# Kernel optimization log

Measured on AMD Instinct MI355X. Metric: run time of the kernel, lower is better.

Reference implementation:

```python
import jax, jax.numpy as jnp
import numpy as np

B, S, H, NH = 2, 2048, 1024, 16
HD = H // NH  # head_dim = 64
ROPE_BASE = 10000.0


def _rope(x):
    # x: [B, NH, S, HD]; LLaMA-style half-split rotary embedding
    s, d = x.shape[2], x.shape[3]
    inv_freq = 1.0 / (ROPE_BASE ** (jnp.arange(0, d, 2, dtype=jnp.float32) / d))  # [d/2]
    ang = jnp.arange(s, dtype=jnp.float32)[:, None] * inv_freq[None, :]            # [S, d/2]
    cos, sin = jnp.cos(ang), jnp.sin(ang)
    x1, x2 = x[..., : d // 2], x[..., d // 2:]
    return jnp.concatenate([x1 * cos - x2 * sin, x1 * sin + x2 * cos], axis=-1)


def setup_inputs() -> dict:
    key = jax.random.key(0)
    ks = jax.random.split(key, 9)
    hidden_states = jax.random.normal(ks[0], (B, S, H), dtype=jnp.float32)
    # causal mask: True = attend
    causal = jnp.tril(jnp.ones((S, S), dtype=bool))
    attention_mask = jnp.broadcast_to(causal[None, None, :, :], (B, 1, S, S))
    std = 0.02
    wq = jax.random.normal(ks[1], (H, NH * HD), dtype=jnp.float32) * std
    wk = jax.random.normal(ks[2], (H, NH * HD), dtype=jnp.float32) * std
    wv = jax.random.normal(ks[3], (H, NH * HD), dtype=jnp.float32) * std
    wo = jax.random.normal(ks[4], (NH * HD, H), dtype=jnp.float32) * std
    bq = jnp.zeros((NH * HD,), dtype=jnp.float32)
    bk = jnp.zeros((NH * HD,), dtype=jnp.float32)
    bv = jnp.zeros((NH * HD,), dtype=jnp.float32)
    bo = jnp.zeros((H,), dtype=jnp.float32)
    return {"hidden_states": hidden_states, "attention_mask": attention_mask,
            "wq": wq, "bq": bq, "wk": wk, "bk": bk, "wv": wv, "bv": bv,
            "wo": wo, "bo": bo}


def _split_heads(x):
    b, s, _ = x.shape
    return jnp.transpose(x.reshape(b, s, NH, HD), (0, 2, 1, 3))


def reference(hidden_states, attention_mask, wq, bq, wk, bk, wv, bv, wo, bo):
    q = _split_heads(hidden_states @ wq + bq)  # [B,NH,S,HD]
    k = _split_heads(hidden_states @ wk + bk)
    v = _split_heads(hidden_states @ wv + bv)
    q = _rope(q)
    k = _rope(k)
    scores = jnp.einsum('bhqd,bhkd->bhqk', q, k) / jnp.sqrt(jnp.float32(HD))
    scores = jnp.where(attention_mask, scores, jnp.float32(-1e9))
    weights = jax.nn.softmax(scores, axis=-1)
    attn = jnp.einsum('bhqk,bhkv->bhqv', weights, v)  # [B,NH,S,HD]
    attn = jnp.transpose(attn, (0, 2, 1, 3)).reshape(hidden_states.shape[0], attn.shape[2], H)
    return attn @ wo + bo
```

## Files before the change

kernel.cpp:

```cpp
#include <hip/hip_runtime.h>
#include <math.h>

typedef short bf16x8 __attribute__((ext_vector_type(8)));
typedef short bf16x4 __attribute__((ext_vector_type(4)));
typedef float f32x4  __attribute__((ext_vector_type(4)));

__device__ __forceinline__ unsigned short f2bf(float f) {
    union { float f; unsigned u; } v; v.f = f;
    unsigned r = v.u + 0x7FFFu + ((v.u >> 16) & 1u);
    return (unsigned short)(r >> 16);
}

__device__ __forceinline__ unsigned cvt_pk_bf16(float a, float b) {
    unsigned r;
    asm("v_cvt_pk_bf16_f32 %0, %1, %2" : "=v"(r) : "v"(a), "v"(b));
    return r;
}

#define GLDS16(gp, lp) __builtin_amdgcn_global_load_lds( \
    (const __attribute__((address_space(1))) void*)(gp), \
    (__attribute__((address_space(3))) void*)(lp), 16, 0, 0)


__global__ __launch_bounds__(256)
void prep(const float* __restrict__ X, unsigned short* __restrict__ Xb,
          const float* __restrict__ w0, const float* __restrict__ w1,
          const float* __restrict__ w2, const float* __restrict__ w3,
          unsigned short* o0, unsigned short* o1,
          unsigned short* o2, unsigned short* o3)
{
    const int z = blockIdx.z;
    if (z >= 4) {
        const int lb = (z - 4) * 256 + blockIdx.y * 16 + blockIdx.x;
        const size_t t = (size_t)lb * 256 + threadIdx.x;
        const float4 a = *(const float4*)(X + t * 8);
        const float4 b = *(const float4*)(X + t * 8 + 4);
        unsigned short u[8] = { f2bf(a.x), f2bf(a.y), f2bf(a.z), f2bf(a.w),
                                f2bf(b.x), f2bf(b.y), f2bf(b.z), f2bf(b.w) };
        *(int4*)(Xb + t * 8) = *(int4*)u;
        return;
    }
    const float* W; unsigned short* O;
    switch (z) {
        case 0: W = w0; O = o0; break;
        case 1: W = w1; O = o1; break;
        case 2: W = w2; O = o2; break;
        default: W = w3; O = o3; break;
    }
    __shared__ float T[64][65];
    const int tid = threadIdx.x;
    const int n0 = blockIdx.x * 64, k0 = blockIdx.y * 64;
    #pragma unroll
    for (int i = 0; i < 4; i++) {
        const int k = (tid >> 4) + i * 16, n4 = (tid & 15) * 4;
        const float4 v = *(const float4*)(W + (size_t)(k0 + k) * 1024 + n0 + n4);
        T[k][n4] = v.x; T[k][n4+1] = v.y; T[k][n4+2] = v.z; T[k][n4+3] = v.w;
    }
    __syncthreads();
    if (z == 3) {
        #pragma unroll
        for (int i = 0; i < 4; i++) {
            const int n = (tid >> 4) + i * 16, k4 = (tid & 15) * 4;
            unsigned short u[4];
            #pragma unroll
            for (int j = 0; j < 4; j++) {
                const int q = k4 + j;
                const int p = (q & 3) * 16 + (q >> 2);
                const int d = (p & 3) * 16 + (p >> 2);
                u[j] = f2bf(T[d][n]);
            }
            *(int2*)(O + (size_t)(n0 + n) * 1024 + k0 + k4) = *(int2*)u;
        }
    } else {
        #pragma unroll
        for (int i = 0; i < 4; i++) {
            const int n = (tid >> 4) + i * 16, k4 = (tid & 15) * 4;
            unsigned short u[4] = { f2bf(T[k4][n]), f2bf(T[k4+1][n]),
                                    f2bf(T[k4+2][n]), f2bf(T[k4+3][n]) };
            *(int2*)(O + (size_t)(n0 + n) * 1024 + k0 + k4) = *(int2*)u;
        }
    }
}

__global__ __launch_bounds__(256)
void qkv_gemm(const unsigned short* __restrict__ Xb,
              const unsigned short* __restrict__ Wtq, const unsigned short* __restrict__ Wtk,
              const unsigned short* __restrict__ Wtv,
              const float* __restrict__ bq, const float* __restrict__ bk,
              const float* __restrict__ bv,
              unsigned short* __restrict__ Qb, unsigned short* __restrict__ Kb,
              unsigned short* __restrict__ Vtb)
{
    const unsigned short* Wt; const float* bias; unsigned short* Out;
    const int z = blockIdx.z;
    if (z == 0)      { Wt = Wtq; bias = bq; Out = Qb; }
    else if (z == 1) { Wt = Wtk; bias = bk; Out = Kb; }
    else             { Wt = Wtv; bias = bv; Out = Vtb; }

    __shared__ unsigned short Sh[16384];
    unsigned short* T = Sh;

    const int tid = threadIdx.x, lane = tid & 63, w = tid >> 6;
    const int quad = lane >> 4, c = lane & 15;
    const int wr = w >> 1, wc = w & 1;
    const int m0 = blockIdx.x * 128, n0 = blockIdx.y * 128;
    const int srow = lane >> 2;
    const int scol = ((lane & 3) ^ ((lane >> 3) & 3)) * 8;
    const int sA = (quad ^ ((c >> 1) & 3)) * 8;

    f32x4 acc[4][4];
    #pragma unroll
    for (int i = 0; i < 4; i++)
        #pragma unroll
        for (int j = 0; j < 4; j++) acc[i][j] = (f32x4){0.f, 0.f, 0.f, 0.f};

    #pragma unroll
    for (int j = 0; j < 2; j++) {
        const int r = w * 32 + j * 16;
        GLDS16(Xb + (size_t)(m0 + r + srow) * 1024 + 0 + scol, &Sh[r * 32]);
        GLDS16(Wt + (size_t)(n0 + r + srow) * 1024 + 0 + scol, &Sh[4096 + r * 32]);
    }
    __syncthreads();

    int cur = 0;
    for (int t = 0; t < 32; ++t) {
        if (t + 1 < 32) {
            const int kn = (t + 1) * 32;
            unsigned short* An = Sh + (cur ^ 1) * 8192;
            unsigned short* Bn = An + 4096;
            #pragma unroll
            for (int j = 0; j < 2; j++) {
                const int r = w * 32 + j * 16;
                GLDS16(Xb + (size_t)(m0 + r + srow) * 1024 + kn + scol, &An[r * 32]);
                GLDS16(Wt + (size_t)(n0 + r + srow) * 1024 + kn + scol, &Bn[r * 32]);
            }
        }
        const unsigned short* As = Sh + cur * 8192;
        const unsigned short* Bs = As + 4096;
        bf16x8 af[4], bf[4];
        #pragma unroll
        for (int rt = 0; rt < 4; rt++)
            af[rt] = *(const bf16x8*)&As[(wr * 64 + rt * 16 + c) * 32 + sA];
        #pragma unroll
        for (int nt = 0; nt < 4; nt++)
            bf[nt] = *(const bf16x8*)&Bs[(wc * 64 + nt * 16 + c) * 32 + sA];
        #pragma unroll
        for (int rt = 0; rt < 4; rt++)
            #pragma unroll
            for (int nt = 0; nt < 4; nt++)
                acc[rt][nt] = __builtin_amdgcn_mfma_f32_16x16x32_bf16(af[rt], bf[nt], acc[rt][nt], 0, 0, 0);
        __syncthreads();
        cur ^= 1;
    }

    float bv4[4];
    #pragma unroll
    for (int nt = 0; nt < 4; nt++) bv4[nt] = bias[n0 + wc * 64 + nt * 16 + c];

    if (z == 2) {
        const int b = m0 >> 11, sb = m0 & 2047;
        const int hgbase = n0 >> 6;
        #pragma unroll
        for (int h = 0; h < 2; h++) {
            if (wc == h) {
                #pragma unroll
                for (int rt = 0; rt < 4; rt++)
                    #pragma unroll
                    for (int reg = 0; reg < 4; reg++) {
                        const int s = wr * 64 + rt * 16 + quad * 4 + reg;
                        unsigned short u[4];
                        #pragma unroll
                        for (int nt = 0; nt < 4; nt++)
                            u[nt] = f2bf(acc[rt][nt][reg] + bv4[nt]);
                        *(int2*)&T[s * 72 + c * 4] = *(int2*)u;
                    }
            }
            __syncthreads();
            const int p = tid >> 2, s8 = (tid & 3) * 32;
            unsigned short* dstb = Vtb + ((size_t)(b * 16 + hgbase + h) * 64 + p) * 2048 + sb;
            #pragma unroll
            for (int jj = 0; jj < 32; jj += 8) {
                unsigned short u[8];
                #pragma unroll
                for (int j = 0; j < 8; j++) u[j] = T[(s8 + jj + j) * 72 + p];
                *(int4*)(dstb + s8 + jj) = *(int4*)u;
            }
            __syncthreads();
        }
        return;
    }

    const float kLn = 9.210340371976184f / 32.0f;
    const float TWO_PI_INV = 0.15915494309189535f;
    const float rv0 = expf(-(float)c * kLn) * TWO_PI_INV;
    const float rv1 = expf(-(float)(c + 16) * kLn) * TWO_PI_INV;
    const float qscale = (z == 0) ? 0.125f : 1.0f;

    #pragma unroll
    for (int rt = 0; rt < 4; rt++) {
        #pragma unroll
        for (int reg = 0; reg < 4; reg++) {
            const int m = m0 + wr * 64 + rt * 16 + quad * 4 + reg;
            const int b = m >> 11, s = m & 2047;
            float x0 = acc[rt][0][reg] + bv4[0];
            float x1 = acc[rt][1][reg] + bv4[1];
            float x2 = acc[rt][2][reg] + bv4[2];
            float x3 = acc[rt][3][reg] + bv4[3];
            float r0 = (float)s * rv0;  r0 -= floorf(r0);
            float r1 = (float)s * rv1;  r1 -= floorf(r1);
            const float sn0 = __builtin_amdgcn_sinf(r0);
            const float cs0 = __builtin_amdgcn_cosf(r0);
            const float sn1 = __builtin_amdgcn_sinf(r1);
            const float cs1 = __builtin_amdgcn_cosf(r1);
            const float y0 = (x0 * cs0 - x2 * sn0) * qscale;
            const float y2 = (x0 * sn0 + x2 * cs0) * qscale;
            const float y1 = (x1 * cs1 - x3 * sn1) * qscale;
            const float y3 = (x1 * sn1 + x3 * cs1) * qscale;
            const int h = (n0 + wc * 64) >> 6;
            unsigned short u[4] = { f2bf(y0), f2bf(y1), f2bf(y2), f2bf(y3) };
            unsigned short* dst = Out + ((size_t)(b * 16 + h) * 2048 + s) * 64;
            *(int2*)(dst + c * 4) = *(int2*)u;
        }
    }
}

__global__ __launch_bounds__(256)
void out_gemm(const unsigned short* __restrict__ Ab, const unsigned short* __restrict__ Wto,
              const float* __restrict__ bo, float* __restrict__ Out)
{
    __shared__ unsigned short As[64 * 32];
    __shared__ unsigned short Bs[128 * 32];
    const int tid = threadIdx.x, lane = tid & 63, w = tid >> 6;
    const int quad = lane >> 4, c = lane & 15;
    const int wr = w >> 1, wc = w & 1;
    const int m0 = blockIdx.x * 64, n0 = blockIdx.y * 128;
    const int srow = lane >> 2, scol = (lane & 3) * 8;

    f32x4 acc[2][4];
    #pragma unroll
    for (int i = 0; i < 2; i++)
        #pragma unroll
        for (int j = 0; j < 4; j++) acc[i][j] = (f32x4){0.f, 0.f, 0.f, 0.f};

    for (int k0 = 0; k0 < 1024; k0 += 32) {
        {
            const int r = w * 16;
            GLDS16(Ab + (size_t)(m0 + r + srow) * 1024 + k0 + scol, &As[r * 32]);
        }
        #pragma unroll
        for (int j = 0; j < 2; j++) {
            const int r = w * 32 + j * 16;
            GLDS16(Wto + (size_t)(n0 + r + srow) * 1024 + k0 + scol, &Bs[r * 32]);
        }
        __syncthreads();
        bf16x8 af[2], bf[4];
        #pragma unroll
        for (int rt = 0; rt < 2; rt++)
            af[rt] = *(const bf16x8*)&As[(wr * 32 + rt * 16 + c) * 32 + quad * 8];
        #pragma unroll
        for (int nt = 0; nt < 4; nt++)
            bf[nt] = *(const bf16x8*)&Bs[(wc * 64 + nt * 16 + c) * 32 + quad * 8];
        #pragma unroll
        for (int rt = 0; rt < 2; rt++)
            #pragma unroll
            for (int nt = 0; nt < 4; nt++)
                acc[rt][nt] = __builtin_amdgcn_mfma_f32_16x16x32_bf16(af[rt], bf[nt], acc[rt][nt], 0, 0, 0);
        __syncthreads();
    }
    #pragma unroll
    for (int rt = 0; rt < 2; rt++) {
        #pragma unroll
        for (int reg = 0; reg < 4; reg++) {
            const int m = m0 + wr * 32 + rt * 16 + quad * 4 + reg;
            #pragma unroll
            for (int nt = 0; nt < 4; nt++) {
                const int n = n0 + wc * 64 + nt * 16 + c;
                Out[(size_t)m * 1024 + n] = acc[rt][nt][reg] + bo[n];
            }
        }
    }
}

__global__ __launch_bounds__(512)
void attn_part(const unsigned short* __restrict__ Qb, const unsigned short* __restrict__ Kb,
               const unsigned short* __restrict__ Vtb, unsigned short* __restrict__ Ab,
               float* __restrict__ Opart, float* __restrict__ Lpart)
{
    __shared__ unsigned short Ks[64 * 72];
    __shared__ unsigned short Vs[64 * 72];

    const int tid = threadIdx.x, w = tid >> 6, lane = tid & 63;
    const int quad = lane >> 4, c = lane & 15;
    const int bh = blockIdx.y;
    const int x = blockIdx.x;
    const int i = (int)((0x014425566377ULL >> (4 * x)) & 15);
    const int chunk = (594 >> x) & 1;
    const int len = ((i >= 4) ? 2 : 4) * (i + 1);
    const int start = chunk ? len : 0;
    const int q0 = i * 256;
    const bool complete = (i <= 3);
    const size_t base = (size_t)bh * 2048 * 64;

    bf16x8 on;
    #pragma unroll
    for (int ii = 0; ii < 8; ii++) on[ii] = (short)0x3F80;

    const int qbase = q0 + w * 32;
    const size_t qoffA = base + (size_t)(qbase + c) * 64;
    const size_t qoffB = base + (size_t)(qbase + 16 + c) * 64;
    const bf16x8 qfA0 = *(const bf16x8*)(Qb + qoffA + quad * 8);
    const bf16x8 qfA1 = *(const bf16x8*)(Qb + qoffA + 32 + quad * 8);
    const bf16x8 qfB0 = *(const bf16x8*)(Qb + qoffB + quad * 8);
    const bf16x8 qfB1 = *(const bf16x8*)(Qb + qoffB + 32 + quad * 8);

    f32x4 OA[4], OB[4], OsA, OsB;
    OsA = (f32x4){0.f, 0.f, 0.f, 0.f};
    OsB = (f32x4){0.f, 0.f, 0.f, 0.f};
    #pragma unroll
    for (int nt = 0; nt < 4; nt++) { OA[nt] = OsA; OB[nt] = OsA; }

    const int rs = tid >> 3, c8 = (tid & 7) * 8;

    int k0 = start * 64;
    int4 kreg = *(const int4*)(Kb  + base + (size_t)(k0 + rs) * 64 + c8);
    int4 vreg = *(const int4*)(Vtb + base + (size_t)rs * 2048 + k0 + c8);

    union P8 { bf16x8 v8; unsigned wd[4]; };
    union V8 { bf16x8 v8; bf16x4 v4[2]; };

    for (int t = 0; t < len; t++, k0 += 64) {
        *(int4*)&Ks[(size_t)rs * 72 + c8] = kreg;
        *(int4*)&Vs[(size_t)rs * 72 + c8] = vreg;
        __syncthreads();

        if (t + 1 < len) {
            const int kn = k0 + 64;
            kreg = *(const int4*)(Kb  + base + (size_t)(kn + rs) * 64 + c8);
            vreg = *(const int4*)(Vtb + base + (size_t)rs * 2048 + kn + c8);
        }

        if (k0 <= qbase + 31) {
            const int qrowA = qbase + c;
            const int qrowB = qbase + 16 + c;
            const bool nmA = (k0 + 63) > qbase;
            const bool nmB = (k0 + 63) > (qbase + 16);
            P8 paA0, paA1, paB0, paB1;
            __builtin_amdgcn_s_setprio(1);
            #pragma unroll
            for (int nt = 0; nt < 4; nt++) {
                const bf16x8 kf0 = *(const bf16x8*)&Ks[(nt * 16 + c) * 72 + quad * 8];
                const bf16x8 kf1 = *(const bf16x8*)&Ks[(nt * 16 + c) * 72 + 32 + quad * 8];
                f32x4 sA = (f32x4){0.f, 0.f, 0.f, 0.f};
                f32x4 sB = sA;
                sA = __builtin_amdgcn_mfma_f32_16x16x32_bf16(kf0, qfA0, sA, 0, 0, 0);
                sA = __builtin_amdgcn_mfma_f32_16x16x32_bf16(kf1, qfA1, sA, 0, 0, 0);
                sB = __builtin_amdgcn_mfma_f32_16x16x32_bf16(kf0, qfB0, sB, 0, 0, 0);
                sB = __builtin_amdgcn_mfma_f32_16x16x32_bf16(kf1, qfB1, sB, 0, 0, 0);
                const int keyb = k0 + nt * 16 + quad * 4;
                float pA[4], pB[4];
                #pragma unroll
                for (int reg = 0; reg < 4; reg++) {
                    float va = __expf(sA[reg]);
                    if (nmA && (keyb + reg > qrowA)) va = 0.f;
                    pA[reg] = va;
                    float vb = __expf(sB[reg]);
                    if (nmB && (keyb + reg > qrowB)) vb = 0.f;
                    pB[reg] = vb;
                }
                const unsigned waA = cvt_pk_bf16(pA[0], pA[1]);
                const unsigned wbA = cvt_pk_bf16(pA[2], pA[3]);
                const unsigned waB = cvt_pk_bf16(pB[0], pB[1]);
                const unsigned wbB = cvt_pk_bf16(pB[2], pB[3]);
                if (nt < 2) {
                    paA0.wd[2 * nt] = waA;     paA0.wd[2 * nt + 1] = wbA;
                    paB0.wd[2 * nt] = waB;     paB0.wd[2 * nt + 1] = wbB;
                } else {
                    paA1.wd[2 * (nt-2)] = waA; paA1.wd[2 * (nt-2) + 1] = wbA;
                    paB1.wd[2 * (nt-2)] = waB; paB1.wd[2 * (nt-2) + 1] = wbB;
                }
            }

            #pragma unroll
            for (int nt = 0; nt < 4; nt++) {
                const int pr = (nt * 16 + c) * 72 + 4 * quad;
                V8 vb0, vb1;
                vb0.v4[0] = *(const bf16x4*)&Vs[pr];
                vb0.v4[1] = *(const bf16x4*)&Vs[pr + 16];
                vb1.v4[0] = *(const bf16x4*)&Vs[pr + 32];
                vb1.v4[1] = *(const bf16x4*)&Vs[pr + 48];
                OA[nt] = __builtin_amdgcn_mfma_f32_16x16x32_bf16(paA0.v8, vb0.v8, OA[nt], 0, 0, 0);
                OA[nt] = __builtin_amdgcn_mfma_f32_16x16x32_bf16(paA1.v8, vb1.v8, OA[nt], 0, 0, 0);
                OB[nt] = __builtin_amdgcn_mfma_f32_16x16x32_bf16(paB0.v8, vb0.v8, OB[nt], 0, 0, 0);
                OB[nt] = __builtin_amdgcn_mfma_f32_16x16x32_bf16(paB1.v8, vb1.v8, OB[nt], 0, 0, 0);
            }
            OsA = __builtin_amdgcn_mfma_f32_16x16x32_bf16(paA0.v8, on, OsA, 0, 0, 0);
            OsA = __builtin_amdgcn_mfma_f32_16x16x32_bf16(paA1.v8, on, OsA, 0, 0, 0);
            OsB = __builtin_amdgcn_mfma_f32_16x16x32_bf16(paB0.v8, on, OsB, 0, 0, 0);
            OsB = __builtin_amdgcn_mfma_f32_16x16x32_bf16(paB1.v8, on, OsB, 0, 0, 0);
            __builtin_amdgcn_s_setprio(0);
        }
        __syncthreads();
    }

    if (complete) {
        const int b = bh >> 4, h = bh & 15;
        #pragma unroll
        for (int reg = 0; reg < 4; reg++) {
            const float invA = 1.0f / OsA[reg];
            const int qA = qbase + quad * 4 + reg;
            unsigned short uA[4];
            #pragma unroll
            for (int nt = 0; nt < 4; nt++) uA[nt] = f2bf(OA[nt][reg] * invA);
            unsigned short* dA = Ab + ((size_t)(b * 2048 + qA)) * 1024 + h * 64;
            *(int2*)(dA + c * 4) = *(int2*)uA;

            const float invB = 1.0f / OsB[reg];
            const int qB = qbase + 16 + quad * 4 + reg;
            unsigned short uB[4];
            #pragma unroll
            for (int nt = 0; nt < 4; nt++) uB[nt] = f2bf(OB[nt][reg] * invB);
            unsigned short* dB = Ab + ((size_t)(b * 2048 + qB)) * 1024 + h * 64;
            *(int2*)(dB + c * 4) = *(int2*)uB;
        }
    } else {
        const int slot = (i - 4) * 2 + chunk;
        float* Op = Opart + ((size_t)bh * 8 + slot) * 16384;
        float* Lp = Lpart + (size_t)bh * 2048 + (size_t)slot * 256;
        #pragma unroll
        for (int reg = 0; reg < 4; reg++) {
            const int rowA = w * 32 + quad * 4 + reg;
            float4 oA = make_float4(OA[0][reg], OA[1][reg], OA[2][reg], OA[3][reg]);
            *(float4*)(Op + (size_t)rowA * 64 + c * 4) = oA;
            if (c == 0) Lp[rowA] = OsA[reg];

            const int rowB = rowA + 16;
            float4 oB = make_float4(OB[0][reg], OB[1][reg], OB[2][reg], OB[3][reg]);
            *(float4*)(Op + (size_t)rowB * 64 + c * 4) = oB;
            if (c == 0) Lp[rowB] = OsB[reg];
        }
    }
}

__global__ __launch_bounds__(256)
void attn_combine(const float* __restrict__ Opart, const float* __restrict__ Lpart,
                  unsigned short* __restrict__ Ab)
{
    const int tid = threadIdx.x;
    const int j = blockIdx.x, bh = blockIdx.y;
    const int i = 4 + (j >> 1), half = j & 1;
    const int slot0 = (i - 4) * 2;
    const int q0 = i * 256 + half * 128;
    const size_t s0 = ((size_t)bh * 8 + slot0) * 16384 + (size_t)half * 128 * 64;
    const size_t l0 = (size_t)bh * 2048 + (size_t)slot0 * 256 + half * 128;

    __shared__ float linv[128];
    if (tid < 128) linv[tid] = 1.0f / (Lpart[l0 + tid] + Lpart[l0 + 256 + tid]);
    __syncthreads();

    const int row = tid >> 1, col0 = (tid & 1) * 32;
    const float inv = linv[row];
    const int b = bh >> 4, h = bh & 15;
    const int q = q0 + row;
    unsigned short* dst = Ab + ((size_t)(b * 2048 + q)) * 1024 + h * 64 + col0;
    #pragma unroll
    for (int c4 = 0; c4 < 32; c4 += 4) {
        const float4 a  = *(const float4*)(Opart + s0 + (size_t)row * 64 + col0 + c4);
        const float4 bb = *(const float4*)(Opart + s0 + 16384 + (size_t)row * 64 + col0 + c4);
        dst[c4 + 0] = f2bf((a.x + bb.x) * inv);
        dst[c4 + 1] = f2bf((a.y + bb.y) * inv);
        dst[c4 + 2] = f2bf((a.z + bb.z) * inv);
        dst[c4 + 3] = f2bf((a.w + bb.w) * inv);
    }
}

extern "C" void kernel_launch(void* const* d_in, const int* in_sizes, int n_in,
                              void* d_out, int out_size, void* d_ws, size_t ws_size,
                              hipStream_t stream)
{
    const float* X  = (const float*)d_in[0];
    const float* wq = (const float*)d_in[2];
    const float* bq = (const float*)d_in[3];
    const float* wk = (const float*)d_in[4];
    const float* bk = (const float*)d_in[5];
    const float* wv = (const float*)d_in[6];
    const float* bv = (const float*)d_in[7];
    const float* wo = (const float*)d_in[8];
    const float* bo = (const float*)d_in[9];

    unsigned short* ws = (unsigned short*)d_ws;
    const size_t M1 = 1024 * 1024;
    unsigned short* Xb  = ws;
    unsigned short* Wtq = Xb  + 4 * M1;
    unsigned short* Wtk = Wtq + M1;
    unsigned short* Wtv = Wtk + M1;
    unsigned short* Wto = Wtv + M1;
    unsigned short* Qb  = Wto + M1;
    unsigned short* Kb  = Qb  + 4 * M1;
    unsigned short* Vtb = Kb  + 4 * M1;
    unsigned short* Ab  = Vtb + 4 * M1;
    float* Opart = (float*)(Ab + 4 * M1);
    float* Lpart = Opart + (size_t)32 * 8 * 16384;

    prep        <<<dim3(16, 16, 12), 256, 0, stream>>>(X, Xb, wq, wk, wv, wo,
                                                       Wtq, Wtk, Wtv, Wto);
    qkv_gemm    <<<dim3(32, 8, 3), 256, 0, stream>>>(Xb, Wtq, Wtk, Wtv, bq, bk, bv,
                                                     Qb, Kb, Vtb);
    attn_part   <<<dim3(12, 32), 512, 0, stream>>>(Qb, Kb, Vtb, Ab, Opart, Lpart);
    attn_combine<<<dim3(8, 32), 256, 0, stream>>>(Opart, Lpart, Ab);
    out_gemm    <<<dim3(64, 8), 256, 0, stream>>>(Ab, Wto, bo, (float*)d_out);
}
```

Before: 212.7 us.

## Double-buffer attention K/V tiles via direct global-to-LDS loads with XOR swizzle

Replaces the register-staged K/V prefetch in attn_part with global_load_lds directly into a double-buffered LDS tile. A row-XOR swizzle replaces the padded stride of 72. The loop now needs one barrier per tile instead of two, and the next tile's load overlaps the current tile's MFMA work without using registers. The cost is doubled LDS use per block and reliance on the barrier to order the asynchronous LDS writes.

Result: slower. 235.9 us (+10.9%).

```diff
diff --git a/kernel.cpp b/kernel.cpp
--- a/kernel.cpp
+++ b/kernel.cpp
@@ -286,8 +286,8 @@
                const unsigned short* __restrict__ Vtb, unsigned short* __restrict__ Ab,
                float* __restrict__ Opart, float* __restrict__ Lpart)
 {
-    __shared__ unsigned short Ks[64 * 72];
-    __shared__ unsigned short Vs[64 * 72];
+    __shared__ unsigned short Ks[2][64 * 64];
+    __shared__ unsigned short Vs[2][64 * 64];
 
     const int tid = threadIdx.x, w = tid >> 6, lane = tid & 63;
     const int quad = lane >> 4, c = lane & 15;
@@ -319,24 +319,25 @@
     #pragma unroll
     for (int nt = 0; nt < 4; nt++) { OA[nt] = OsA; OB[nt] = OsA; }
 
-    const int rs = tid >> 3, c8 = (tid & 7) * 8;
-
-    int k0 = start * 64;
-    int4 kreg = *(const int4*)(Kb  + base + (size_t)(k0 + rs) * 64 + c8);
-    int4 vreg = *(const int4*)(Vtb + base + (size_t)rs * 2048 + k0 + c8);
-
+    const int srow = tid >> 3, sp7 = tid & 7;
+    const int sls  = sp7 ^ (srow & 7);
+    const unsigned short* Ksrc = Kb  + base + (size_t)srow * 64   + sls * 8;
+    const unsigned short* Vsrc = Vtb + base + (size_t)srow * 2048 + sls * 8;
+
+    const int c7 = c & 7;
     union P8 { bf16x8 v8; unsigned wd[4]; };
     union V8 { bf16x8 v8; bf16x4 v4[2]; };
 
+    int k0 = start * 64;
+    GLDS16(Ksrc + (size_t)k0 * 64, &Ks[0][tid * 8]);
+    GLDS16(Vsrc + k0,              &Vs[0][tid * 8]);
+    __syncthreads();
+
+    int cur = 0;
     for (int t = 0; t < len; t++, k0 += 64) {
-        *(int4*)&Ks[(size_t)rs * 72 + c8] = kreg;
-        *(int4*)&Vs[(size_t)rs * 72 + c8] = vreg;
-        __syncthreads();
-
         if (t + 1 < len) {
-            const int kn = k0 + 64;
-            kreg = *(const int4*)(Kb  + base + (size_t)(kn + rs) * 64 + c8);
-            vreg = *(const int4*)(Vtb + base + (size_t)rs * 2048 + kn + c8);
+            GLDS16(Ksrc + (size_t)(k0 + 64) * 64, &Ks[cur ^ 1][tid * 8]);
+            GLDS16(Vsrc + (k0 + 64),              &Vs[cur ^ 1][tid * 8]);
         }
 
         if (k0 <= qbase + 31) {
@@ -348,8 +349,9 @@
             __builtin_amdgcn_s_setprio(1);
             #pragma unroll
             for (int nt = 0; nt < 4; nt++) {
-                const bf16x8 kf0 = *(const bf16x8*)&Ks[(nt * 16 + c) * 72 + quad * 8];
-                const bf16x8 kf1 = *(const bf16x8*)&Ks[(nt * 16 + c) * 72 + 32 + quad * 8];
+                const int krow = (nt * 16 + c) * 64;
+                const bf16x8 kf0 = *(const bf16x8*)&Ks[cur][krow + ((quad ^ c7) * 8)];
+                const bf16x8 kf1 = *(const bf16x8*)&Ks[cur][krow + (((quad + 4) ^ c7) * 8)];
                 f32x4 sA = (f32x4){0.f, 0.f, 0.f, 0.f};
                 f32x4 sB = sA;
                 sA = __builtin_amdgcn_mfma_f32_16x16x32_bf16(kf0, qfA0, sA, 0, 0, 0);
@@ -380,14 +382,15 @@
                 }
             }
 
+            const int q1 = quad >> 1, hh = (quad & 1) * 4;
             #pragma unroll
             for (int nt = 0; nt < 4; nt++) {
-                const int pr = (nt * 16 + c) * 72 + 4 * quad;
+                const int vrow = (nt * 16 + c) * 64;
                 V8 vb0, vb1;
-                vb0.v4[0] = *(const bf16x4*)&Vs[pr];
-                vb0.v4[1] = *(const bf16x4*)&Vs[pr + 16];
-                vb1.v4[0] = *(const bf16x4*)&Vs[pr + 32];
-                vb1.v4[1] = *(const bf16x4*)&Vs[pr + 48];
+                vb0.v4[0] = *(const bf16x4*)&Vs[cur][vrow + (((q1 + 0) ^ c7) * 8) + hh];
+                vb0.v4[1] = *(const bf16x4*)&Vs[cur][vrow + (((q1 + 2) ^ c7) * 8) + hh];
+                vb1.v4[0] = *(const bf16x4*)&Vs[cur][vrow + (((q1 + 4) ^ c7) * 8) + hh];
+                vb1.v4[1] = *(const bf16x4*)&Vs[cur][vrow + (((q1 + 6) ^ c7) * 8) + hh];
                 OA[nt] = __builtin_amdgcn_mfma_f32_16x16x32_bf16(paA0.v8, vb0.v8, OA[nt], 0, 0, 0);
                 OA[nt] = __builtin_amdgcn_mfma_f32_16x16x32_bf16(paA1.v8, vb1.v8, OA[nt], 0, 0, 0);
                 OB[nt] = __builtin_amdgcn_mfma_f32_16x16x32_bf16(paB0.v8, vb0.v8, OB[nt], 0, 0, 0);
@@ -400,6 +403,7 @@
             __builtin_amdgcn_s_setprio(0);
         }
         __syncthreads();
+        cur ^= 1;
     }
 
     if (complete) {
```

## Rebalance causal attention split-KV work with table-driven block decomposition

Applied to the files above, without the earlier changes.

Attention work splitting moves from 12 blocks per head to 20, driven by a constant table that packs each block's query tile, KV start, length, partial slot and completeness flag. Query tiles 2 through 7 are now split into 2, 3 or 4 KV chunks, and the combine kernel sums a variable number of partials. The goal is to even out per-block work under the causal mask and raise occupancy across the CUs. In exchange it writes and reads more fp32 partial outputs, and the combine kernel handles 12 tiles instead of 8.

Result: slower. 229.8 us (+8.0%).

```diff
diff --git a/kernel.cpp b/kernel.cpp
--- a/kernel.cpp
+++ b/kernel.cpp
@@ -21,6 +21,18 @@
     (const __attribute__((address_space(1))) void*)(gp), \
     (__attribute__((address_space(3))) void*)(lp), 16, 0, 0)
 
+
+__device__ const unsigned XT[20] = {
+    59399u, 63559u, 67719u, 71879u,
+    30725u, 34885u, 39045u,
+    10243u, 14403u,
+    133121u,
+    42758u, 46910u, 51062u, 55214u,
+    18180u, 22332u,
+    26228u,
+    1538u, 5682u,
+    132096u
+};
 
 __global__ __launch_bounds__(256)
 void prep(const float* __restrict__ X, unsigned short* __restrict__ Xb,
@@ -292,13 +304,13 @@
     const int tid = threadIdx.x, w = tid >> 6, lane = tid & 63;
     const int quad = lane >> 4, c = lane & 15;
     const int bh = blockIdx.y;
-    const int x = blockIdx.x;
-    const int i = (int)((0x014425566377ULL >> (4 * x)) & 15);
-    const int chunk = (594 >> x) & 1;
-    const int len = ((i >= 4) ? 2 : 4) * (i + 1);
-    const int start = chunk ? len : 0;
+    const unsigned e = XT[blockIdx.x];
+    const int i     = e & 7;
+    const int start = (e >> 3) & 31;
+    const int len   = (e >> 8) & 15;
+    const int slot  = (e >> 12) & 31;
+    const bool complete = (e >> 17) & 1;
     const int q0 = i * 256;
-    const bool complete = (i <= 3);
     const size_t base = (size_t)bh * 2048 * 64;
 
     bf16x8 on;
@@ -423,9 +435,8 @@
             *(int2*)(dB + c * 4) = *(int2*)uB;
         }
     } else {
-        const int slot = (i - 4) * 2 + chunk;
-        float* Op = Opart + ((size_t)bh * 8 + slot) * 16384;
-        float* Lp = Lpart + (size_t)bh * 2048 + (size_t)slot * 256;
+        float* Op = Opart + ((size_t)bh * 18 + slot) * 16384;
+        float* Lp = Lpart + ((size_t)bh * 18 + slot) * 256;
         #pragma unroll
         for (int reg = 0; reg < 4; reg++) {
             const int rowA = w * 32 + quad * 4 + reg;
@@ -447,14 +458,19 @@
 {
     const int tid = threadIdx.x;
     const int j = blockIdx.x, bh = blockIdx.y;
-    const int i = 4 + (j >> 1), half = j & 1;
-    const int slot0 = (i - 4) * 2;
+    const int i = 2 + (j >> 1), half = j & 1;
+    const int sb = (i < 4) ? 2 * (i - 2) : ((i < 6) ? 3 * i - 8 : 4 * i - 14);
+    const int n  = (i < 4) ? 2 : ((i < 6) ? 3 : 4);
     const int q0 = i * 256 + half * 128;
-    const size_t s0 = ((size_t)bh * 8 + slot0) * 16384 + (size_t)half * 128 * 64;
-    const size_t l0 = (size_t)bh * 2048 + (size_t)slot0 * 256 + half * 128;
+    const size_t s0 = ((size_t)bh * 18 + sb) * 16384 + (size_t)half * 128 * 64;
+    const size_t l0 = ((size_t)bh * 18 + sb) * 256 + half * 128;
 
     __shared__ float linv[128];
-    if (tid < 128) linv[tid] = 1.0f / (Lpart[l0 + tid] + Lpart[l0 + 256 + tid]);
+    if (tid < 128) {
+        float l = 0.f;
+        for (int s = 0; s < n; s++) l += Lpart[l0 + (size_t)s * 256 + tid];
+        linv[tid] = 1.0f / l;
+    }
     __syncthreads();
 
     const int row = tid >> 1, col0 = (tid & 1) * 32;
@@ -464,12 +480,15 @@
     unsigned short* dst = Ab + ((size_t)(b * 2048 + q)) * 1024 + h * 64 + col0;
     #pragma unroll
     for (int c4 = 0; c4 < 32; c4 += 4) {
-        const float4 a  = *(const float4*)(Opart + s0 + (size_t)row * 64 + col0 + c4);
-        const float4 bb = *(const float4*)(Opart + s0 + 16384 + (size_t)row * 64 + col0 + c4);
-        dst[c4 + 0] = f2bf((a.x + bb.x) * inv);
-        dst[c4 + 1] = f2bf((a.y + bb.y) * inv);
-        dst[c4 + 2] = f2bf((a.z + bb.z) * inv);
-        dst[c4 + 3] = f2bf((a.w + bb.w) * inv);
+        float4 a = *(const float4*)(Opart + s0 + (size_t)row * 64 + col0 + c4);
+        for (int s = 1; s < n; s++) {
+            const float4 bb = *(const float4*)(Opart + s0 + (size_t)s * 16384 + (size_t)row * 64 + col0 + c4);
+            a.x += bb.x; a.y += bb.y; a.z += bb.z; a.w += bb.w;
+        }
+        dst[c4 + 0] = f2bf(a.x * inv);
+        dst[c4 + 1] = f2bf(a.y * inv);
+        dst[c4 + 2] = f2bf(a.z * inv);
+        dst[c4 + 3] = f2bf(a.w * inv);
     }
 }
 
@@ -499,13 +518,13 @@
     unsigned short* Vtb = Kb  + 4 * M1;
     unsigned short* Ab  = Vtb + 4 * M1;
     float* Opart = (float*)(Ab + 4 * M1);
-    float* Lpart = Opart + (size_t)32 * 8 * 16384;
+    float* Lpart = Opart + (size_t)32 * 18 * 16384;
 
     prep        <<<dim3(16, 16, 12), 256, 0, stream>>>(X, Xb, wq, wk, wv, wo,
                                                        Wtq, Wtk, Wtv, Wto);
     qkv_gemm    <<<dim3(32, 8, 3), 256, 0, stream>>>(Xb, Wtq, Wtk, Wtv, bq, bk, bv,
                                                      Qb, Kb, Vtb);
-    attn_part   <<<dim3(12, 32), 512, 0, stream>>>(Qb, Kb, Vtb, Ab, Opart, Lpart);
-    attn_combine<<<dim3(8, 32), 256, 0, stream>>>(Opart, Lpart, Ab);
+    attn_part   <<<dim3(20, 32), 512, 0, stream>>>(Qb, Kb, Vtb, Ab, Opart, Lpart);
+    attn_combine<<<dim3(12, 32), 256, 0, stream>>>(Opart, Lpart, Ab);
     out_gemm    <<<dim3(64, 8), 256, 0, stream>>>(Ab, Wto, bo, (float*)d_out);
 }
```
